# Kernel tuning notes

Hardware: AMD Instinct MI355X
Metric: run time of the kernel (lower is better)

## Reference

```python
import jax, jax.numpy as jnp
import numpy as np

BS, D_IN, D_OUT, N_MASKS = 1024, 512, 512, 8

def setup_inputs() -> dict:
    key = jax.random.key(0)
    k1, k2, k3, k4 = jax.random.split(key, 4)
    x = jax.random.normal(k1, (BS, D_IN), dtype=jnp.float32)
    state = jax.random.randint(k2, (BS,), 0, N_MASKS, dtype=jnp.int32)
    # glorot-uniform-like kernel
    limit = float(np.sqrt(6.0 / (D_IN + D_OUT)))
    kernel = jax.random.uniform(k3, (D_IN, D_OUT), dtype=jnp.float32, minval=-limit, maxval=limit)
    # binary MADE connectivity masks (0/1)
    masks = (jax.random.uniform(k4, (N_MASKS, D_IN, D_OUT)) < 0.5).astype(jnp.float32)
    return {"x": x, "state": state, "kernel": kernel, "masks": masks}

def reference(x, state, kernel, masks):
    # Math of original: out = relu(x[b] @ (kernel * masks[state[b]]))
    # Efficient form: precompute all n masked kernels (small n), batched matmul,
    # then gather per-sample result. Avoids materializing [bs, d_in, d_out].
    masked = kernel[None, :, :] * masks            # [n, d_in, d_out]
    y_all = jnp.einsum('bi,nio->bno', x, masked)   # [bs, n, d_out]
    y = jnp.take_along_axis(y_all, state[:, None, None].astype(jnp.int32), axis=1)[:, 0, :]
    return jax.nn.relu(y)
```

## Files before the change

### kernel.cpp

```cpp
#include <hip/hip_runtime.h>

#define BS 1024
#define D_IN 512
#define D_OUT 512
#define N_MASKS 8

typedef short bf16x8 __attribute__((ext_vector_type(8)));
typedef float f32x4 __attribute__((ext_vector_type(4)));

#define WF_OFF_USH (8192 / 2)
#define WF_USH     (N_MASKS * 16 * 32 * 512)
#define XB_OFF_USH (WF_OFF_USH + WF_USH)

__device__ __forceinline__ ushort f2bf(float f) {
    union { float f; unsigned u; } x; x.f = f;
    unsigned r = (x.u + 0x7fffu + ((x.u >> 16) & 1u)) >> 16;
    return (ushort)r;
}

__global__ void __launch_bounds__(256) prep_kernel(
    const float* __restrict__ x, const int* __restrict__ state,
    const float* __restrict__ kern, const float* __restrict__ masks,
    int* __restrict__ wsi, ushort* __restrict__ wf, ushort* __restrict__ xb)
{
    const int bx  = blockIdx.x;
    const int tid = threadIdx.x;

    if (bx < 1024) {
        const int n  = bx >> 7;
        const int kb = (bx >> 3) & 15;
        const int cb = (bx & 7) * 4 + (tid >> 6);
        const int l  = tid & 63;
        const int g  = l >> 4;
        const int cl = l & 15;
        const int k0  = kb * 32 + g * 8;
        const int col = cb * 16 + cl;
        const float* kp = kern + (size_t)k0 * D_OUT + col;
        const float* mp = masks + (size_t)n * (D_IN * D_OUT) + (size_t)k0 * D_OUT + col;
        uint pk[4];
        #pragma unroll
        for (int j = 0; j < 4; ++j) {
            float v0 = kp[(2*j)   * D_OUT] * mp[(2*j)   * D_OUT];
            float v1 = kp[(2*j+1) * D_OUT] * mp[(2*j+1) * D_OUT];
            pk[j] = (uint)f2bf(v0) | ((uint)f2bf(v1) << 16);
        }
        uint4 o; o.x = pk[0]; o.y = pk[1]; o.z = pk[2]; o.w = pk[3];
        *(uint4*)(wf + ((size_t)((n * 16 + kb) * 32 + cb)) * 512 + l * 8) = o;
    } else if (bx < 1280) {
        const int idx = (bx - 1024) * 256 + tid;
        const float4 a = ((const float4*)x)[idx * 2];
        const float4 b = ((const float4*)x)[idx * 2 + 1];
        uint4 o;
        o.x = (uint)f2bf(a.x) | ((uint)f2bf(a.y) << 16);
        o.y = (uint)f2bf(a.z) | ((uint)f2bf(a.w) << 16);
        o.z = (uint)f2bf(b.x) | ((uint)f2bf(b.y) << 16);
        o.w = (uint)f2bf(b.z) | ((uint)f2bf(b.w) << 16);
        *(uint4*)(xb + (size_t)idx * 8) = o;
    } else {
        __shared__ int cnt[N_MASKS];
        __shared__ int offs[N_MASKS + 1];
        if (tid < N_MASKS) cnt[tid] = 0;
        __syncthreads();
        int s[4];
        #pragma unroll
        for (int r = 0; r < 4; ++r) {
            s[r] = state[r * 256 + tid];
            atomicAdd(&cnt[s[r]], 1);
        }
        __syncthreads();
        if (tid == 0) {
            int acc = 0;
            for (int i = 0; i < N_MASKS; ++i) { offs[i] = acc; acc += cnt[i]; }
            offs[N_MASKS] = acc;
        }
        __syncthreads();
        if (tid <= N_MASKS) wsi[tid] = offs[tid];
        if (tid < N_MASKS) cnt[tid] = offs[tid];
        __syncthreads();
        #pragma unroll
        for (int r = 0; r < 4; ++r) {
            const int pos = atomicAdd(&cnt[s[r]], 1);
            wsi[16 + pos] = r * 256 + tid;
        }
    }
}

__global__ void __launch_bounds__(256) gemm_kernel(
    const ushort* __restrict__ xb, const ushort* __restrict__ wf,
    const int* __restrict__ wsi, float* __restrict__ out)
{
    const int n  = blockIdx.x;
    const int rt = blockIdx.z;

    const int off0 = wsi[n];
    const int off1 = wsi[n + 1];
    if (rt * 16 >= off1 - off0) return;

    __shared__ int ridx[16];
    const int tid = threadIdx.x;
    if (tid < 16) {
        const int p = off0 + rt * 16 + tid;
        ridx[tid] = (p < off1) ? wsi[16 + p] : -1;
    }
    __syncthreads();

    const int lane = tid & 63;
    const int wid  = tid >> 6;
    const int g    = lane >> 4;
    const int cl   = lane & 15;

    const int myrow = ridx[cl];
    const ushort* xrow = xb + (size_t)(myrow < 0 ? 0 : myrow) * D_IN + g * 8;
    const int cf = blockIdx.y * 4 + wid;
    const ushort* wp = wf + ((size_t)(n * 16) * 32 + cf) * 512 + lane * 8;

    f32x4 accE = {0.f, 0.f, 0.f, 0.f};
    f32x4 accO = {0.f, 0.f, 0.f, 0.f};

    #pragma unroll
    for (int kb = 0; kb < 16; kb += 2) {
        const bf16x8 a0 = *(const bf16x8*)(xrow + kb * 32);
        const bf16x8 a1 = *(const bf16x8*)(xrow + (kb + 1) * 32);
        const bf16x8 b0 = *(const bf16x8*)(wp + (size_t)kb * 32 * 512);
        const bf16x8 b1 = *(const bf16x8*)(wp + (size_t)(kb + 1) * 32 * 512);
        accE = __builtin_amdgcn_mfma_f32_16x16x32_bf16(a0, b0, accE, 0, 0, 0);
        accO = __builtin_amdgcn_mfma_f32_16x16x32_bf16(a1, b1, accO, 0, 0, 0);
    }

    #pragma unroll
    for (int r = 0; r < 4; ++r) {
        const int b = ridx[g * 4 + r];
        if (b >= 0) {
            out[(size_t)b * D_OUT + cf * 16 + cl] = fmaxf(accE[r] + accO[r], 0.f);
        }
    }
}

extern "C" void kernel_launch(void* const* d_in, const int* in_sizes, int n_in,
                              void* d_out, int out_size, void* d_ws, size_t ws_size,
                              hipStream_t stream) {
    const float* x     = (const float*)d_in[0];
    const int*   state = (const int*)d_in[1];
    const float* kern  = (const float*)d_in[2];
    const float* masks = (const float*)d_in[3];
    float*  out = (float*)d_out;
    int*    wsi = (int*)d_ws;
    ushort* wsu = (ushort*)d_ws;

    prep_kernel<<<1281, 256, 0, stream>>>(x, state, kern, masks,
                                          wsi, wsu + WF_OFF_USH, wsu + XB_OFF_USH);
    dim3 grid(N_MASKS, D_OUT / 64, BS / 16);
    gemm_kernel<<<grid, 256, 0, stream>>>(wsu + XB_OFF_USH, wsu + WF_OFF_USH, wsi, out);
}
```

Baseline: 19.08 us.

## Fuse masked-weight prep into GEMM via LDS and convert x inline

Result: slower. 24.40 us (+27.9%).

```diff
diff --git a/kernel.cpp b/kernel.cpp
--- a/kernel.cpp
+++ b/kernel.cpp
@@ -4,13 +4,11 @@
 #define D_IN 512
 #define D_OUT 512
 #define N_MASKS 8
+#define CB 16
 
 typedef short bf16x8 __attribute__((ext_vector_type(8)));
 typedef float f32x4 __attribute__((ext_vector_type(4)));
 
-#define WF_OFF_USH (8192 / 2)
-#define WF_USH     (N_MASKS * 16 * 32 * 512)
-#define XB_OFF_USH (WF_OFF_USH + WF_USH)
 
 __device__ __forceinline__ ushort f2bf(float f) {
     union { float f; unsigned u; } x; x.f = f;
@@ -18,120 +16,100 @@
     return (ushort)r;
 }
 
-__global__ void __launch_bounds__(256) prep_kernel(
-    const float* __restrict__ x, const int* __restrict__ state,
-    const float* __restrict__ kern, const float* __restrict__ masks,
-    int* __restrict__ wsi, ushort* __restrict__ wf, ushort* __restrict__ xb)
+__device__ __forceinline__ bf16x8 pack8(float4 a0, float4 a1) {
+    union { uint u[4]; bf16x8 v; } r;
+    r.u[0] = (uint)f2bf(a0.x) | ((uint)f2bf(a0.y) << 16);
+    r.u[1] = (uint)f2bf(a0.z) | ((uint)f2bf(a0.w) << 16);
+    r.u[2] = (uint)f2bf(a1.x) | ((uint)f2bf(a1.y) << 16);
+    r.u[3] = (uint)f2bf(a1.z) | ((uint)f2bf(a1.w) << 16);
+    return r.v;
+}
+
+__global__ void __launch_bounds__(BS) sort_kernel(const int* __restrict__ state,
+                                                  int* __restrict__ wsi) {
+    __shared__ int cnt[N_MASKS];
+    __shared__ int offs[N_MASKS + 1];
+    const int tid = threadIdx.x;
+    if (tid < N_MASKS) cnt[tid] = 0;
+    __syncthreads();
+    const int s = state[tid];
+    atomicAdd(&cnt[s], 1);
+    __syncthreads();
+    if (tid == 0) {
+        int acc = 0;
+        for (int i = 0; i < N_MASKS; ++i) { offs[i] = acc; acc += cnt[i]; }
+        offs[N_MASKS] = acc;
+    }
+    __syncthreads();
+    if (tid <= N_MASKS) wsi[tid] = offs[tid];
+    if (tid < N_MASKS) cnt[tid] = offs[tid];
+    __syncthreads();
+    const int pos = atomicAdd(&cnt[s], 1);
+    wsi[16 + pos] = tid;
+}
+
+__global__ void __launch_bounds__(512) fused_kernel(
+    const float* __restrict__ x, const float* __restrict__ kern,
+    const float* __restrict__ masks, const int* __restrict__ wsi,
+    float* __restrict__ out)
 {
-    const int bx  = blockIdx.x;
+    __shared__ ushort wlds[16 * 64 * 8];
+    const int n   = blockIdx.x;
+    const int cb0 = blockIdx.y * CB;
     const int tid = threadIdx.x;
+    const float* __restrict__ maskn = masks + (size_t)n * (D_IN * D_OUT);
 
-    if (bx < 1024) {
-        const int n  = bx >> 7;
-        const int kb = (bx >> 3) & 15;
-        const int cb = (bx & 7) * 4 + (tid >> 6);
-        const int l  = tid & 63;
+    #pragma unroll
+    for (int it = 0; it < 2; ++it) {
+        const int slot = it * 512 + tid;
+        const int kb = slot >> 6;
+        const int l  = slot & 63;
         const int g  = l >> 4;
         const int cl = l & 15;
-        const int k0  = kb * 32 + g * 8;
-        const int col = cb * 16 + cl;
-        const float* kp = kern + (size_t)k0 * D_OUT + col;
-        const float* mp = masks + (size_t)n * (D_IN * D_OUT) + (size_t)k0 * D_OUT + col;
+        const int kbase = kb * 32 + g * 8;
+        const float* kp = kern  + (size_t)kbase * D_OUT + cb0 + cl;
+        const float* mp = maskn + (size_t)kbase * D_OUT + cb0 + cl;
         uint pk[4];
         #pragma unroll
-        for (int j = 0; j < 4; ++j) {
-            float v0 = kp[(2*j)   * D_OUT] * mp[(2*j)   * D_OUT];
-            float v1 = kp[(2*j+1) * D_OUT] * mp[(2*j+1) * D_OUT];
-            pk[j] = (uint)f2bf(v0) | ((uint)f2bf(v1) << 16);
+        for (int h = 0; h < 4; ++h) {
+            const float v0 = kp[(2*h)   * D_OUT] * mp[(2*h)   * D_OUT];
+            const float v1 = kp[(2*h+1) * D_OUT] * mp[(2*h+1) * D_OUT];
+            pk[h] = (uint)f2bf(v0) | ((uint)f2bf(v1) << 16);
         }
         uint4 o; o.x = pk[0]; o.y = pk[1]; o.z = pk[2]; o.w = pk[3];
-        *(uint4*)(wf + ((size_t)((n * 16 + kb) * 32 + cb)) * 512 + l * 8) = o;
-    } else if (bx < 1280) {
-        const int idx = (bx - 1024) * 256 + tid;
-        const float4 a = ((const float4*)x)[idx * 2];
-        const float4 b = ((const float4*)x)[idx * 2 + 1];
-        uint4 o;
-        o.x = (uint)f2bf(a.x) | ((uint)f2bf(a.y) << 16);
-        o.y = (uint)f2bf(a.z) | ((uint)f2bf(a.w) << 16);
-        o.z = (uint)f2bf(b.x) | ((uint)f2bf(b.y) << 16);
-        o.w = (uint)f2bf(b.z) | ((uint)f2bf(b.w) << 16);
-        *(uint4*)(xb + (size_t)idx * 8) = o;
-    } else {
-        __shared__ int cnt[N_MASKS];
-        __shared__ int offs[N_MASKS + 1];
-        if (tid < N_MASKS) cnt[tid] = 0;
-        __syncthreads();
-        int s[4];
-        #pragma unroll
-        for (int r = 0; r < 4; ++r) {
-            s[r] = state[r * 256 + tid];
-            atomicAdd(&cnt[s[r]], 1);
-        }
-        __syncthreads();
-        if (tid == 0) {
-            int acc = 0;
-            for (int i = 0; i < N_MASKS; ++i) { offs[i] = acc; acc += cnt[i]; }
-            offs[N_MASKS] = acc;
-        }
-        __syncthreads();
-        if (tid <= N_MASKS) wsi[tid] = offs[tid];
-        if (tid < N_MASKS) cnt[tid] = offs[tid];
-        __syncthreads();
-        #pragma unroll
-        for (int r = 0; r < 4; ++r) {
-            const int pos = atomicAdd(&cnt[s[r]], 1);
-            wsi[16 + pos] = r * 256 + tid;
-        }
+        *(uint4*)&wlds[slot * 8] = o;
     }
-}
-
-__global__ void __launch_bounds__(256) gemm_kernel(
-    const ushort* __restrict__ xb, const ushort* __restrict__ wf,
-    const int* __restrict__ wsi, float* __restrict__ out)
-{
-    const int n  = blockIdx.x;
-    const int rt = blockIdx.z;
+    __syncthreads();
 
     const int off0 = wsi[n];
     const int off1 = wsi[n + 1];
-    if (rt * 16 >= off1 - off0) return;
-
-    __shared__ int ridx[16];
-    const int tid = threadIdx.x;
-    if (tid < 16) {
-        const int p = off0 + rt * 16 + tid;
-        ridx[tid] = (p < off1) ? wsi[16 + p] : -1;
-    }
-    __syncthreads();
-
+    const int gcnt = off1 - off0;
     const int lane = tid & 63;
     const int wid  = tid >> 6;
     const int g    = lane >> 4;
     const int cl   = lane & 15;
 
-    const int myrow = ridx[cl];
-    const ushort* xrow = xb + (size_t)(myrow < 0 ? 0 : myrow) * D_IN + g * 8;
-    const int cf = blockIdx.y * 4 + wid;
-    const ushort* wp = wf + ((size_t)(n * 16) * 32 + cf) * 512 + lane * 8;
+    for (int rt = wid; rt * 16 < gcnt; rt += 8) {
+        const int p  = off0 + rt * 16 + cl;
+        const int rv = (p < off1) ? wsi[16 + p] : -1;
+        const float* xr = x + (size_t)(rv < 0 ? 0 : rv) * D_IN + g * 8;
 
-    f32x4 accE = {0.f, 0.f, 0.f, 0.f};
-    f32x4 accO = {0.f, 0.f, 0.f, 0.f};
+        f32x4 acc = {0.f, 0.f, 0.f, 0.f};
+        #pragma unroll
+        for (int kb = 0; kb < 16; ++kb) {
+            const float4 a0 = *(const float4*)(xr + kb * 32);
+            const float4 a1 = *(const float4*)(xr + kb * 32 + 4);
+            const bf16x8 a  = pack8(a0, a1);
+            const bf16x8 b  = *(const bf16x8*)&wlds[(kb * 64 + lane) * 8];
+            acc = __builtin_amdgcn_mfma_f32_16x16x32_bf16(a, b, acc, 0, 0, 0);
+        }
 
-    #pragma unroll
-    for (int kb = 0; kb < 16; kb += 2) {
-        const bf16x8 a0 = *(const bf16x8*)(xrow + kb * 32);
-        const bf16x8 a1 = *(const bf16x8*)(xrow + (kb + 1) * 32);
-        const bf16x8 b0 = *(const bf16x8*)(wp + (size_t)kb * 32 * 512);
-        const bf16x8 b1 = *(const bf16x8*)(wp + (size_t)(kb + 1) * 32 * 512);
-        accE = __builtin_amdgcn_mfma_f32_16x16x32_bf16(a0, b0, accE, 0, 0, 0);
-        accO = __builtin_amdgcn_mfma_f32_16x16x32_bf16(a1, b1, accO, 0, 0, 0);
-    }
-
-    #pragma unroll
-    for (int r = 0; r < 4; ++r) {
-        const int b = ridx[g * 4 + r];
-        if (b >= 0) {
-            out[(size_t)b * D_OUT + cf * 16 + cl] = fmaxf(accE[r] + accO[r], 0.f);
+        #pragma unroll
+        for (int r = 0; r < 4; ++r) {
+            const int brow = __shfl(rv, g * 4 + r);
+            if (brow >= 0) {
+                out[(size_t)brow * D_OUT + cb0 + cl] = fmaxf(acc[r], 0.f);
+            }
         }
     }
 }
@@ -143,12 +121,10 @@
     const int*   state = (const int*)d_in[1];
     const float* kern  = (const float*)d_in[2];
     const float* masks = (const float*)d_in[3];
-    float*  out = (float*)d_out;
-    int*    wsi = (int*)d_ws;
-    ushort* wsu = (ushort*)d_ws;
+    float* out = (float*)d_out;
+    int*   wsi = (int*)d_ws;
 
-    prep_kernel<<<1281, 256, 0, stream>>>(x, state, kern, masks,
-                                          wsi, wsu + WF_OFF_USH, wsu + XB_OFF_USH);
-    dim3 grid(N_MASKS, D_OUT / 64, BS / 16);
-    gemm_kernel<<<grid, 256, 0, stream>>>(wsu + XB_OFF_USH, wsu + WF_OFF_USH, wsi, out);
+    sort_kernel<<<1, BS, 0, stream>>>(state, wsi);
+    dim3 grid(N_MASKS, D_OUT / CB);
+    fused_kernel<<<grid, 512, 0, stream>>>(x, kern, masks, wsi, out);
 }
```
